# Optimization experiments

Hardware: AMD Instinct MI355X
Metric: run time of the kernel (lower is better)

Reference implementation:

```python
import jax, jax.numpy as jnp
import numpy as np

H = 2048
I = 8192
E = 8
EI = I // E  # expert_intermediate_size = 1024


def setup_inputs() -> dict:
    key = jax.random.key(0)
    k1, k2, k3 = jax.random.split(key, 3)
    B, N = 4, 4096
    x = jax.random.normal(k1, (B, N, H), dtype=jnp.float32)
    position_ids = jnp.arange(B * N, dtype=jnp.int64).reshape(B, N)
    gate_up_proj = 0.02 * jax.random.normal(k2, (E, H, EI * 2), dtype=jnp.float32)
    down_proj = 0.02 * jax.random.normal(k3, (E, EI, H), dtype=jnp.float32)
    return {"x": x, "position_ids": position_ids,
            "gate_up_proj": gate_up_proj, "down_proj": down_proj}


def reference(x, position_ids, gate_up_proj, down_proj):
    # x: [B,N,H]; position_ids: [B,N] (or [N]); expert = pos % E.
    B, N, Hdim = x.shape
    if position_ids.ndim == 1:
        position_ids = jnp.broadcast_to(position_ids[None, :], (B, N))
    eids = (position_ids % E).reshape(B * N)
    flat = x.reshape(B * N, Hdim)

    # Modulo routing is perfectly balanced (N % E == 0 with sequential ids),
    # so group tokens by expert (stable sort) and run dense per-expert GEMMs
    # instead of per-token gathered-weight bmm (same math, no weight blowup).
    T = B * N
    order = jnp.argsort(eids)          # stable in jax -> tokens grouped by expert
    xg = flat[order].reshape(E, T // E, Hdim)            # [E, T/E, H]
    gu = jnp.einsum('ebh,ehk->ebk', xg, gate_up_proj)    # [E, T/E, 2*EI]
    gate, up = gu[..., :EI], gu[..., EI:]
    inter = jax.nn.silu(gate) * up                       # [E, T/E, EI]
    outg = jnp.einsum('ebi,eih->ebh', inter, down_proj)  # [E, T/E, H]
    out = jnp.zeros((T, Hdim), dtype=x.dtype).at[order].set(outg.reshape(T, Hdim))
    return out.reshape(B, N, Hdim)
```

## Files before the change

### kernel.cpp

```cpp
#include <hip/hip_runtime.h>
#include <hip/hip_bf16.h>

typedef unsigned short u16;
typedef __attribute__((ext_vector_type(8))) short short8;
typedef __attribute__((ext_vector_type(8))) unsigned short u16x8;
typedef __attribute__((ext_vector_type(4))) float f32x4;

#define H_DIM 2048
#define EI_DIM 1024
#define NEXP 8

template <int V> struct IC { static constexpr int value = V; };

__device__ __forceinline__ u16 f2bf(float f) {
  __hip_bfloat16 h = __float2bfloat16(f);
  return __builtin_bit_cast(unsigned short, h);
}

__device__ __forceinline__ void load_lds16(const void* g, void* lds) {
  __builtin_amdgcn_global_load_lds(
      (const __attribute__((address_space(1))) unsigned int*)g,
      (__attribute__((address_space(3))) unsigned int*)lds, 16, 0, 0);
}

__global__ void hist_kernel(const int* __restrict__ pid, int* __restrict__ hist) {
  int seg = blockIdx.x, lane = threadIdx.x;
  int eid = pid[seg * 64 + lane] & 7;
#pragma unroll
  for (int e = 0; e < NEXP; ++e) {
    unsigned long long m = __ballot(eid == e);
    if (lane == 0) hist[e * 256 + seg] = __popcll(m);
  }
}

__global__ void scan_kernel(const int* __restrict__ hist, int* __restrict__ base,
                            int* __restrict__ offcnt, int T) {
  __shared__ int lds[256];
  int tid = threadIdx.x;
  int v[8], s = 0;
#pragma unroll
  for (int j = 0; j < 8; ++j) { v[j] = hist[tid * 8 + j]; s += v[j]; }
  lds[tid] = s;
  __syncthreads();
  for (int d = 1; d < 256; d <<= 1) {
    int t = (tid >= d) ? lds[tid - d] : 0;
    __syncthreads();
    lds[tid] += t;
    __syncthreads();
  }
  int run = lds[tid] - s;
#pragma unroll
  for (int j = 0; j < 8; ++j) { base[tid * 8 + j] = run; run += v[j]; }
  __syncthreads();
  if (tid < NEXP) {
    int o = base[tid * 256];
    int nx = (tid < NEXP - 1) ? base[(tid + 1) * 256] : T;
    offcnt[tid] = o;
    offcnt[8 + tid] = nx - o;
  }
}

__global__ void rank_kernel(const int* __restrict__ pid, const int* __restrict__ base,
                            int* __restrict__ order) {
  int seg = blockIdx.x, lane = threadIdx.x;
  int t = seg * 64 + lane;
  int eid = pid[t] & 7;
  unsigned long long below = (1ull << lane) - 1ull;
#pragma unroll
  for (int e = 0; e < NEXP; ++e) {
    unsigned long long m = __ballot(eid == e);
    if (eid == e) {
      int r = __popcll(m & below);
      order[base[e * 256 + seg] + r] = t;
    }
  }
}

__global__ __launch_bounds__(256) void transpose_bf16(const float* __restrict__ in,
                                                      u16* __restrict__ out, int R, int C) {
  __shared__ u16 tile[64][65];
  int nbr = R >> 6, nbc = C >> 6;
  int per_e = nbr * nbc;
  int bx = blockIdx.x;
  int e = bx / per_e, rem = bx % per_e;
  int tr = rem % nbr, tc = rem / nbr;
  const float* ine = in + (size_t)e * R * C;
  u16* oute = out + (size_t)e * R * C;
  int r0 = tr * 64, c0 = tc * 64;
  int tid = threadIdx.x;
  int lrow = tid >> 4, lc4 = (tid & 15) * 4;
#pragma unroll
  for (int p = 0; p < 4; ++p) {
    int rl = p * 16 + lrow;
    float4 v = *(const float4*)&ine[(size_t)(r0 + rl) * C + c0 + lc4];
    tile[rl][lc4 + 0] = f2bf(v.x);
    tile[rl][lc4 + 1] = f2bf(v.y);
    tile[rl][lc4 + 2] = f2bf(v.z);
    tile[rl][lc4 + 3] = f2bf(v.w);
  }
  __syncthreads();
#pragma unroll
  for (int q = 0; q < 16; ++q) {
    int idx = q * 256 + tid;
    int jr = idx >> 6, hc = idx & 63;
    oute[(size_t)(c0 + jr) * R + r0 + hc] = tile[hc][jr];
  }
}

__global__ __launch_bounds__(256) void gather_x(const float* __restrict__ x,
                                                const int* __restrict__ order,
                                                u16* __restrict__ xg) {
  int g = blockIdx.x;
  int t = order[g];
  const float* src = x + (size_t)t * H_DIM;
  u16* dst = xg + (size_t)g * H_DIM;
  int c = threadIdx.x * 8;
  float4 a = *(const float4*)&src[c];
  float4 b = *(const float4*)&src[c + 4];
  u16x8 v;
  v[0] = f2bf(a.x); v[1] = f2bf(a.y); v[2] = f2bf(a.z); v[3] = f2bf(a.w);
  v[4] = f2bf(b.x); v[5] = f2bf(b.y); v[6] = f2bf(b.z); v[7] = f2bf(b.w);
  *(u16x8*)&dst[c] = v;
}

template <int KTOT, int KIND>
__global__ __launch_bounds__(512, 2) void gemm8_kernel(
    const u16* __restrict__ A, const u16* __restrict__ Bmat, void* __restrict__ outp,
    const int* __restrict__ offcnt, const int* __restrict__ order, int T, int MT) {
  constexpr int NK = KTOT / 64;
  constexpr int ASTR = (KIND == 0) ? H_DIM : EI_DIM;
  constexpr int BSTR = ASTR;
  constexpr size_t BEXP = (size_t)2048 * BSTR;
  __shared__ u16 As[2][2][8192];
  __shared__ u16 Bs[2][2][8192];

  int bx = blockIdx.x;
  int nt = bx & 7;
  int rest = bx >> 3;
  int mt = rest % MT;
  int e = rest / MT;
  int off = offcnt[e], cnt = offcnt[8 + e];
  if (mt * 256 >= cnt) return;

  const u16* Be = Bmat + (size_t)e * BEXP;
  int tid = threadIdx.x, w = tid >> 6, l = tid & 63;
  int wm = w >> 2, wn = w & 3, lr = l & 15, lg = l >> 4;

  const u16* aSrc[2];
  const u16* bSrc[2];
#pragma unroll
  for (int j = 0; j < 2; ++j) {
    int r = j * 128 + (tid >> 2);
    int c = tid & 3;
    int sw = (r >> 1) & 3;
    int grow = min(off + mt * 256 + r, T - 1);
    aSrc[j] = A + (size_t)grow * ASTR + ((c ^ sw) * 8);
    int n;
    if (KIND == 0) {
      int q = r >> 4, rr = r & 15;
      n = ((q & 2) ? EI_DIM : 0) + nt * 128 + ((q >> 2) << 5) + ((q & 1) << 4) + rr;
    } else {
      n = nt * 256 + r;
    }
    bSrc[j] = Be + (size_t)n * BSTR + ((c ^ sw) * 8);
  }

  auto stageA = [&](int kt, int kh, int buf) {
#pragma unroll
    for (int j = 0; j < 2; ++j)
      load_lds16(aSrc[j] + kt * 64 + kh * 32, &As[buf][kh][j * 4096 + w * 512]);
  };
  auto stageB = [&](int kt, int kh, int buf) {
#pragma unroll
    for (int j = 0; j < 2; ++j)
      load_lds16(bSrc[j] + kt * 64 + kh * 32, &Bs[buf][kh][j * 4096 + w * 512]);
  };

  int cidx = (lg ^ ((lr >> 1) & 3)) * 8;
  int aRow0 = wm * 128 + lr;
  int bRow0 = wn * 64 + lr;

  short8 av[4], bv[4];
  auto loadA4 = [&](int buf, int kh, int h) {
#pragma unroll
    for (int mm = 0; mm < 4; ++mm)
      av[mm] = *(const short8*)&As[buf][kh][(aRow0 + (h * 4 + mm) * 16) * 32 + cidx];
  };
  auto loadB4 = [&](int buf, int kh) {
#pragma unroll
    for (int nn = 0; nn < 4; ++nn)
      bv[nn] = *(const short8*)&Bs[buf][kh][(bRow0 + nn * 16) * 32 + cidx];
  };

  f32x4 acc[8][4];
#pragma unroll
  for (int m = 0; m < 8; ++m)
#pragma unroll
    for (int nn = 0; nn < 4; ++nn) acc[m][nn] = {0.f, 0.f, 0.f, 0.f};

  auto MFMA_H = [&](auto HC) {
    constexpr int h = decltype(HC)::value;
    __builtin_amdgcn_s_setprio(1);
#pragma unroll
    for (int mm = 0; mm < 4; ++mm)
#pragma unroll
      for (int nn = 0; nn < 4; ++nn)
        acc[h * 4 + mm][nn] =
            __builtin_amdgcn_mfma_f32_16x16x32_bf16(av[mm], bv[nn], acc[h * 4 + mm][nn], 0, 0, 0);
    __builtin_amdgcn_s_setprio(0);
  };

  stageA(0, 0, 0); stageB(0, 0, 0); stageA(0, 1, 0); stageB(0, 1, 0);
  stageA(1, 0, 1); stageB(1, 0, 1);
  asm volatile("s_waitcnt vmcnt(4)" ::: "memory");
  __builtin_amdgcn_s_barrier();
  __builtin_amdgcn_sched_barrier(0);

  auto TILE = [&](int t, auto BC) {
    constexpr int b = decltype(BC)::value;
    loadA4(b, 0, 0);
    loadB4(b, 0);
    stageA(t + 1, 1, b ^ 1);
    __builtin_amdgcn_s_barrier();
    MFMA_H(IC<0>{});
    __builtin_amdgcn_s_barrier();
    __builtin_amdgcn_sched_barrier(0);
    loadA4(b, 0, 1);
    stageB(t + 1, 1, b ^ 1);
    __builtin_amdgcn_s_barrier();
    MFMA_H(IC<1>{});
    __builtin_amdgcn_s_barrier();
    __builtin_amdgcn_sched_barrier(0);
    loadA4(b, 1, 0);
    loadB4(b, 1);
    stageA(t + 2, 0, b);
    __builtin_amdgcn_s_barrier();
    MFMA_H(IC<0>{});
    __builtin_amdgcn_s_barrier();
    __builtin_amdgcn_sched_barrier(0);
    loadA4(b, 1, 1);
    stageB(t + 2, 0, b);
    __builtin_amdgcn_s_barrier();
    MFMA_H(IC<1>{});
    asm volatile("s_waitcnt vmcnt(4)" ::: "memory");
    __builtin_amdgcn_s_barrier();
    __builtin_amdgcn_sched_barrier(0);
  };

#pragma unroll 1
  for (int t = 0; t < NK - 2; t += 2) {
    TILE(t, IC<0>{});
    TILE(t + 1, IC<1>{});
  }

  {
    constexpr int b = (NK - 2) & 1;
    loadA4(b, 0, 0);
    loadB4(b, 0);
    stageA(NK - 1, 1, b ^ 1);
    MFMA_H(IC<0>{});
    loadA4(b, 0, 1);
    stageB(NK - 1, 1, b ^ 1);
    MFMA_H(IC<1>{});
    loadA4(b, 1, 0);
    loadB4(b, 1);
    MFMA_H(IC<0>{});
    loadA4(b, 1, 1);
    MFMA_H(IC<1>{});
    asm volatile("s_waitcnt vmcnt(0)" ::: "memory");
    __builtin_amdgcn_s_barrier();
    __builtin_amdgcn_sched_barrier(0);
    constexpr int b2 = b ^ 1;
    loadA4(b2, 0, 0);
    loadB4(b2, 0);
    MFMA_H(IC<0>{});
    loadA4(b2, 0, 1);
    MFMA_H(IC<1>{});
    loadA4(b2, 1, 0);
    loadB4(b2, 1);
    MFMA_H(IC<0>{});
    loadA4(b2, 1, 1);
    MFMA_H(IC<1>{});
  }

  if (KIND == 0) {
    u16* inter = (u16*)outp;
#pragma unroll
    for (int m = 0; m < 8; ++m)
#pragma unroll
      for (int nn = 0; nn < 2; ++nn) {
        f32x4 g = acc[m][nn], u = acc[m][nn + 2];
        int icol = nt * 128 + wn * 32 + nn * 16 + lr;
#pragma unroll
        for (int j = 0; j < 4; ++j) {
          int r = wm * 128 + m * 16 + lg * 4 + j;
          int grow = mt * 256 + r;
          if (grow < cnt) {
            float gv = g[j];
            float val = (gv / (1.f + __expf(-gv))) * u[j];
            inter[(size_t)(off + grow) * EI_DIM + icol] = f2bf(val);
          }
        }
      }
  } else {
    float* out = (float*)outp;
#pragma unroll
    for (int m = 0; m < 8; ++m)
#pragma unroll
      for (int nn = 0; nn < 4; ++nn) {
        int ncol = nt * 256 + wn * 64 + nn * 16 + lr;
#pragma unroll
        for (int j = 0; j < 4; ++j) {
          int r = wm * 128 + m * 16 + lg * 4 + j;
          int grow = mt * 256 + r;
          if (grow < cnt) {
            int tt = order[off + grow];
            out[(size_t)tt * H_DIM + ncol] = acc[m][nn][j];
          }
        }
      }
  }
}

extern "C" void kernel_launch(void* const* d_in, const int* in_sizes, int n_in,
                              void* d_out, int out_size, void* d_ws, size_t ws_size,
                              hipStream_t stream) {
  const float* x = (const float*)d_in[0];
  const int* pid = (const int*)d_in[1];
  const float* gup = (const float*)d_in[2];
  const float* dwn = (const float*)d_in[3];
  float* out = (float*)d_out;

  const int T = in_sizes[1];
  const int MT = (T + 255) / 256;

  char* ws = (char*)d_ws;
  size_t o = 0;
  auto take = [&](size_t b) { size_t r = o; o += (b + 255) & ~(size_t)255; return r; };
  int* offcnt = (int*)(ws + take(16 * 4));
  int* hist = (int*)(ws + take(2048 * 4));
  int* base = (int*)(ws + take(2052 * 4));
  int* order = (int*)(ws + take((size_t)T * 4));
  u16* xg = (u16*)(ws + take((size_t)T * H_DIM * 2));
  u16* wguT = (u16*)(ws + take((size_t)NEXP * 2048 * 2048 * 2));
  u16* wdT = (u16*)(ws + take((size_t)NEXP * 2048 * 1024 * 2));
  u16* inter = (u16*)(ws + take((size_t)T * EI_DIM * 2));

  hist_kernel<<<T / 64, 64, 0, stream>>>(pid, hist);
  scan_kernel<<<1, 256, 0, stream>>>(hist, base, offcnt, T);
  rank_kernel<<<T / 64, 64, 0, stream>>>(pid, base, order);
  transpose_bf16<<<NEXP * 32 * 32, 256, 0, stream>>>(gup, wguT, 2048, 2048);
  transpose_bf16<<<NEXP * 16 * 32, 256, 0, stream>>>(dwn, wdT, 1024, 2048);
  gather_x<<<T, 256, 0, stream>>>(x, order, xg);

  gemm8_kernel<2048, 0><<<NEXP * MT * 8, 512, 0, stream>>>(xg, wguT, inter, offcnt, order, T, MT);
  gemm8_kernel<1024, 1><<<NEXP * MT * 8, 512, 0, stream>>>(inter, wdT, out, offcnt, order, T, MT);
}
```

Baseline: 383.6 us.

## Remap workgroups for XCD locality and deepen B-tile prefetch in GEMM pipeline

Workgroup IDs are remapped so that consecutive blocks scheduled round-robin across the 8 XCDs land on tiles sharing the same expert/M rows, aiming at better L2 reuse. The software pipeline is restructured to prefetch both halves of the next B tile earlier, with the vmcnt wait raised from 4 to 6 to match. The epilogue is rewritten with hardcoded buffer indices 0/1, which assumes NK is even and that the loop ends on buffer 0. This adds register and memory-queue pressure and depends on those parity assumptions holding.

```diff
diff --git a/kernel.cpp b/kernel.cpp
--- a/kernel.cpp
+++ b/kernel.cpp
@@ -134,7 +134,10 @@
   __shared__ u16 As[2][2][8192];
   __shared__ u16 Bs[2][2][8192];
 
-  int bx = blockIdx.x;
+  int nwg = gridDim.x;
+  int bid = blockIdx.x;
+  int bx = ((nwg & 7) == 0) ? ((bid & 7) * (nwg >> 3) + (bid >> 3)) : bid;
+
   int nt = bx & 7;
   int rest = bx >> 3;
   int mt = rest % MT;
@@ -211,22 +214,23 @@
   };
 
   stageA(0, 0, 0); stageB(0, 0, 0); stageA(0, 1, 0); stageB(0, 1, 0);
-  stageA(1, 0, 1); stageB(1, 0, 1);
-  asm volatile("s_waitcnt vmcnt(4)" ::: "memory");
+  stageB(1, 0, 1); stageA(1, 0, 1); stageB(1, 1, 1);
+  asm volatile("s_waitcnt vmcnt(6)" ::: "memory");
   __builtin_amdgcn_s_barrier();
   __builtin_amdgcn_sched_barrier(0);
 
   auto TILE = [&](int t, auto BC) {
     constexpr int b = decltype(BC)::value;
+    constexpr int bn = b ^ 1;
     loadA4(b, 0, 0);
     loadB4(b, 0);
-    stageA(t + 1, 1, b ^ 1);
+    stageA(t + 1, 1, bn);
     __builtin_amdgcn_s_barrier();
     MFMA_H(IC<0>{});
     __builtin_amdgcn_s_barrier();
     __builtin_amdgcn_sched_barrier(0);
     loadA4(b, 0, 1);
-    stageB(t + 1, 1, b ^ 1);
+    stageB(t + 2, 0, b);
     __builtin_amdgcn_s_barrier();
     MFMA_H(IC<1>{});
     __builtin_amdgcn_s_barrier();
@@ -239,47 +243,44 @@
     __builtin_amdgcn_s_barrier();
     __builtin_amdgcn_sched_barrier(0);
     loadA4(b, 1, 1);
-    stageB(t + 2, 0, b);
-    __builtin_amdgcn_s_barrier();
-    MFMA_H(IC<1>{});
-    asm volatile("s_waitcnt vmcnt(4)" ::: "memory");
+    stageB(t + 2, 1, b);
+    __builtin_amdgcn_s_barrier();
+    MFMA_H(IC<1>{});
+    asm volatile("s_waitcnt vmcnt(6)" ::: "memory");
     __builtin_amdgcn_s_barrier();
     __builtin_amdgcn_sched_barrier(0);
   };
 
 #pragma unroll 1
-  for (int t = 0; t < NK - 2; t += 2) {
+  for (int t = 0; t < NK - 3; t += 2) {
     TILE(t, IC<0>{});
     TILE(t + 1, IC<1>{});
   }
 
   {
-    constexpr int b = (NK - 2) & 1;
-    loadA4(b, 0, 0);
-    loadB4(b, 0);
-    stageA(NK - 1, 1, b ^ 1);
-    MFMA_H(IC<0>{});
-    loadA4(b, 0, 1);
-    stageB(NK - 1, 1, b ^ 1);
-    MFMA_H(IC<1>{});
-    loadA4(b, 1, 0);
-    loadB4(b, 1);
-    MFMA_H(IC<0>{});
-    loadA4(b, 1, 1);
+    loadA4(0, 0, 0);
+    loadB4(0, 0);
+    stageA(NK - 1, 1, 1);
+    MFMA_H(IC<0>{});
+    loadA4(0, 0, 1);
+    MFMA_H(IC<1>{});
+    loadA4(0, 1, 0);
+    loadB4(0, 1);
+    MFMA_H(IC<0>{});
+    loadA4(0, 1, 1);
     MFMA_H(IC<1>{});
     asm volatile("s_waitcnt vmcnt(0)" ::: "memory");
     __builtin_amdgcn_s_barrier();
     __builtin_amdgcn_sched_barrier(0);
-    constexpr int b2 = b ^ 1;
-    loadA4(b2, 0, 0);
-    loadB4(b2, 0);
-    MFMA_H(IC<0>{});
-    loadA4(b2, 0, 1);
-    MFMA_H(IC<1>{});
-    loadA4(b2, 1, 0);
-    loadB4(b2, 1);
-    MFMA_H(IC<0>{});
-    loadA4(b2, 1, 1);
+    loadA4(1, 0, 0);
+    loadB4(1, 0);
+    MFMA_H(IC<0>{});
+    loadA4(1, 0, 1);
+    MFMA_H(IC<1>{});
+    loadA4(1, 1, 0);
+    loadB4(1, 1);
+    MFMA_H(IC<0>{});
+    loadA4(1, 1, 1);
     MFMA_H(IC<1>{});
   }
 
```

Result: faster. 353.1 us (-8.0%).
